# Kernel optimization log

Measured on AMD Instinct MI355X. Metric: run time of the kernel, lower is better.

## Reference

```python
import jax, jax.numpy as jnp
import numpy as np
import math

B, T, D, H = 2, 2048, 1024, 16
DH = D // H          # 64
NB = DH // 2         # 32 rope blocks
EPS = 1e-5


def _layernorm(x, g, b):
    m = jnp.mean(x, axis=-1, keepdims=True)
    v = jnp.var(x, axis=-1, keepdims=True)
    return (x - m) * jax.lax.rsqrt(v + EPS) * g + b


def _rope(x, cos, sin):
    # x: (B,H,T,DH); cos/sin: (B,H,T,NB)
    x1 = x[..., 0::2]
    x2 = x[..., 1::2]
    o1 = x1 * cos - x2 * sin
    o2 = x1 * sin + x2 * cos
    return jnp.stack([o1, o2], axis=-1).reshape(x.shape)


def setup_inputs() -> dict:
    key = jax.random.key(0)
    ks = jax.random.split(key, 16)
    x = jax.random.normal(ks[0], (B, T, D), dtype=jnp.float32)
    # genuine RoPE angles broadcast to (B,H,T,NB)
    inv_freq = 1.0 / (10000.0 ** (np.arange(NB, dtype=np.float32) / NB))
    ang = jnp.asarray(np.arange(T, dtype=np.float32)[:, None] * inv_freq[None, :])  # (T,NB)
    cos_a = jnp.broadcast_to(jnp.cos(ang)[None, None], (B, H, T, NB)).astype(jnp.float32)
    sin_a = jnp.broadcast_to(jnp.sin(ang)[None, None], (B, H, T, NB)).astype(jnp.float32)
    causal_mask = jnp.triu(jnp.ones((T, T), dtype=bool), k=1)  # True above diagonal -> masked
    s = 0.02
    def w(k, shp):
        return jax.random.normal(k, shp, dtype=jnp.float32) * s
    return {
        "x": x, "cos_a": cos_a, "sin_a": sin_a, "causal_mask": causal_mask,
        "Wq": w(ks[1], (D, D)), "bq": jnp.zeros((D,), jnp.float32),
        "Wk": w(ks[2], (D, D)), "bk": jnp.zeros((D,), jnp.float32),
        "Wv": w(ks[3], (D, D)), "bv": jnp.zeros((D,), jnp.float32),
        "Wo": w(ks[4], (D, D)), "bo": jnp.zeros((D,), jnp.float32),
        "g1": jnp.ones((D,), jnp.float32), "b1n": jnp.zeros((D,), jnp.float32),
        "g2": jnp.ones((D,), jnp.float32), "b2n": jnp.zeros((D,), jnp.float32),
        "W1": w(ks[5], (D, 4 * D)), "bf1": jnp.zeros((4 * D,), jnp.float32),
        "W2": w(ks[6], (4 * D, D)), "bf2": jnp.zeros((D,), jnp.float32),
    }


def reference(x, cos_a, sin_a, causal_mask, Wq, bq, Wk, bk, Wv, bv, Wo, bo,
              g1, b1n, g2, b2n, W1, bf1, W2, bf2):
    h = _layernorm(x, g1, b1n)
    def heads(y):
        return y.reshape(B, T, H, DH).transpose(0, 2, 1, 3)  # (B,H,T,DH)
    Q = heads(h @ Wq + bq)
    K = heads(h @ Wk + bk)
    V = heads(h @ Wv + bv)
    Q = _rope(Q, cos_a, sin_a)
    K = _rope(K, cos_a, sin_a)
    scale = math.sqrt(DH)
    scores = jnp.einsum('bhqd,bhkd->bhqk', Q, K) / scale
    scores = jnp.where(causal_mask[None, None], -jnp.inf, scores)
    attn = jax.nn.softmax(scores, axis=-1)
    out = jnp.einsum('bhqk,bhkd->bhqd', attn, V)
    out = out.transpose(0, 2, 1, 3).reshape(B, T, D)
    out = out @ Wo + bo
    x = x + out  # dropout=0.0 (eval)
    h2 = _layernorm(x, g2, b2n)
    ffn = jax.nn.gelu(h2 @ W1 + bf1, approximate=False) @ W2 + bf2
    return x + ffn
```

## Files before the change

### kernel.cpp

```cpp
#include <hip/hip_runtime.h>

typedef unsigned short u16;
typedef unsigned int   u32;
typedef __attribute__((ext_vector_type(8))) short          short8;
typedef __attribute__((ext_vector_type(4))) float          f32x4;
typedef __attribute__((ext_vector_type(8))) unsigned short u16x8;
typedef __attribute__((ext_vector_type(4))) unsigned short u16x4;

#define T_SEQ  2048
#define DMODEL 1024
#define NHEAD  16
#define DHEAD  64
#define HBUF   4194304

__device__ __forceinline__ float bf2f(u16 u) {
    u32 i = ((u32)u) << 16; float f; __builtin_memcpy(&f, &i, 4); return f;
}
__device__ __forceinline__ u16 f2bf(float f) {
    u32 x; __builtin_memcpy(&x, &f, 4);
    return (u16)((x + 0x7FFFu + ((x >> 16) & 1u)) >> 16);
}

__device__ __forceinline__ void gld16(const u16* g, u16* l) {
    auto gp = reinterpret_cast<const __attribute__((address_space(1))) u32*>(
        reinterpret_cast<uintptr_t>(g));
    auto lp = reinterpret_cast<__attribute__((address_space(3))) u32*>(
        (u32)reinterpret_cast<uintptr_t>(l));
    __builtin_amdgcn_global_load_lds(gp, lp, 16, 0, 0);
}

template<int N> __device__ __forceinline__ void wait_vmcnt() {
    if constexpr (N == 0)      asm volatile("s_waitcnt vmcnt(0)" ::: "memory");
    else if constexpr (N == 3) asm volatile("s_waitcnt vmcnt(3)" ::: "memory");
    else                       asm volatile("s_waitcnt vmcnt(4)" ::: "memory");
}

__global__ __launch_bounds__(256) void ln_k(const float* __restrict__ x,
                                            const float* __restrict__ g,
                                            const float* __restrict__ bb,
                                            u16* __restrict__ out)
{
    int row = blockIdx.x, tid = threadIdx.x;
    const float* xr = x + (size_t)row * DMODEL;
    f32x4 v = *(const f32x4*)(xr + tid * 4);
    float s  = v[0] + v[1] + v[2] + v[3];
    float s2 = v[0]*v[0] + v[1]*v[1] + v[2]*v[2] + v[3]*v[3];
    #pragma unroll
    for (int o = 32; o; o >>= 1) { s += __shfl_xor(s, o); s2 += __shfl_xor(s2, o); }
    __shared__ float rs[4], rq[4];
    if ((tid & 63) == 0) { rs[tid >> 6] = s; rq[tid >> 6] = s2; }
    __syncthreads();
    float S  = rs[0] + rs[1] + rs[2] + rs[3];
    float S2 = rq[0] + rq[1] + rq[2] + rq[3];
    float mean = S * (1.f / DMODEL);
    float var  = S2 * (1.f / DMODEL) - mean * mean;
    float rstd = rsqrtf(var + 1e-5f);
    f32x4 gv = *(const f32x4*)(g + tid * 4);
    f32x4 bv = *(const f32x4*)(bb + tid * 4);
    u16x4 o;
    #pragma unroll
    for (int e = 0; e < 4; e++)
        o[e] = f2bf((v[e] - mean) * rstd * gv[e] + bv[e]);
    *(u16x4*)(out + (size_t)row * DMODEL + tid * 4) = o;
}

__device__ __forceinline__ void tr_body(const float* __restrict__ in,
                                        u16* __restrict__ out, int R, int C,
                                        int bx, int by, int tid)
{
    __shared__ u16 s[64][72];
    int c0 = bx * 64, r0 = by * 64;
    #pragma unroll
    for (int p = 0; p < 2; p++) {
        int r = (tid >> 3) + p * 32, cq = (tid & 7) * 8;
        const float* ip = in + (size_t)(r0 + r) * C + c0 + cq;
        f32x4 a = *(const f32x4*)ip;
        f32x4 b = *(const f32x4*)(ip + 4);
        u16x8 o;
        #pragma unroll
        for (int e = 0; e < 4; e++) { o[e] = f2bf(a[e]); o[4 + e] = f2bf(b[e]); }
        *(u16x8*)(&s[r][cq]) = o;
    }
    __syncthreads();
    int oc = tid >> 2, kq = (tid & 3) * 16;
    u16 tmp[16] __attribute__((aligned(16)));
    #pragma unroll
    for (int e = 0; e < 16; e++) tmp[e] = s[kq + e][oc];
    u16* op = out + (size_t)(c0 + oc) * R + r0 + kq;
    *(u16x8*)op       = *(const u16x8*)(&tmp[0]);
    *(u16x8*)(op + 8) = *(const u16x8*)(&tmp[8]);
}

__global__ __launch_bounds__(256) void trall_k(const float* __restrict__ w0, const float* __restrict__ w1,
                                               const float* __restrict__ w2, const float* __restrict__ w3,
                                               const float* __restrict__ wf1, const float* __restrict__ wf2,
                                               u16* __restrict__ o0, u16* __restrict__ o1,
                                               u16* __restrict__ o2, u16* __restrict__ o3,
                                               u16* __restrict__ of1, u16* __restrict__ of2)
{
    int z = blockIdx.z;
    if (z < 4) {
        const float* in = (z == 0) ? w0 : (z == 1) ? w1 : (z == 2) ? w2 : w3;
        u16* out        = (z == 0) ? o0 : (z == 1) ? o1 : (z == 2) ? o2 : o3;
        tr_body(in, out, 1024, 1024, blockIdx.x, blockIdx.y, threadIdx.x);
    } else if (z < 8) {
        tr_body(wf1, of1, 1024, 4096, blockIdx.x + 16 * (z - 4), blockIdx.y, threadIdx.x);
    } else {
        tr_body(wf2, of2, 4096, 1024, blockIdx.x, blockIdx.y + 16 * (z - 8), threadIdx.x);
    }
}

constexpr int EPI_QKV = 0, EPI_RESF = 1, EPI_GELU = 2, EPI_RES2 = 3;

template<int EPI, int BM>
__global__ __launch_bounds__(256) void gemm_k(
    const u16* __restrict__ A, const u16* __restrict__ Bt, void* __restrict__ outv,
    int M, int N, int K, int Kld,
    const float* __restrict__ b0, const float* __restrict__ b1, const float* __restrict__ b2,
    const float* __restrict__ resid,
    const float* __restrict__ cosp, const float* __restrict__ sinp)
{
    constexpr int MI  = BM / 32;
    constexpr int ASZ = BM * 32, BSZ = 128 * 32;
    constexpr int G   = (BM == 128) ? 4 : 3;
    __shared__ u16 As[3 * ASZ];
    __shared__ u16 Bs[3 * BSZ];
    int tid = threadIdx.x;
    int n0 = blockIdx.x * 128, m0 = blockIdx.y * BM;
    int wave = tid >> 6, lane = tid & 63, lm = lane & 15, ko = lane >> 4;
    int wm = (wave & 1) * (BM / 2), wn = (wave >> 1) * 64;
    f32x4 acc[MI][4];
    #pragma unroll
    for (int i = 0; i < MI; i++)
        #pragma unroll
        for (int j = 0; j < 4; j++) acc[i][j] = (f32x4){0.f, 0.f, 0.f, 0.f};

    int srow = wave * 16 + (lane >> 2);
    int scol = (lane & 3) * 8;
    const u16* Ag = A  + (size_t)(m0 + srow) * Kld + scol;
    const u16* Bg = Bt + (size_t)(n0 + srow) * Kld + scol;
    u16* Al = &As[wave * 16 * 32];
    u16* Bl = &Bs[wave * 16 * 32];

    auto issue = [&](int t, int b) {
        u16* Al2 = Al + b * ASZ;
        u16* Bl2 = Bl + b * BSZ;
        const u16* Ag2 = Ag + t * 32;
        const u16* Bg2 = Bg + t * 32;
        gld16(Ag2, Al2);
        if constexpr (BM == 128) gld16(Ag2 + 64 * (size_t)Kld, Al2 + 64 * 32);
        gld16(Bg2,                    Bl2);
        gld16(Bg2 + 64 * (size_t)Kld, Bl2 + 64 * 32);
    };

    int NT = K >> 5;
    issue(0, 0);
    issue(1, 1);

    int bc = 0, bn = 2;
    for (int kt = 0; kt < NT; kt++) {
        if (kt + 1 < NT) wait_vmcnt<G>();
        else             wait_vmcnt<0>();
        __builtin_amdgcn_s_barrier();
        __builtin_amdgcn_sched_barrier(0);
        if (kt + 2 < NT) issue(kt + 2, bn);

        const u16* Ab = &As[bc * ASZ];
        const u16* Bb = &Bs[bc * BSZ];
        short8 af[MI], bf[4];
        #pragma unroll
        for (int i = 0; i < MI; i++) af[i] = *(const short8*)(&Ab[(wm + i * 16 + lm) * 32 + ko * 8]);
        #pragma unroll
        for (int j = 0; j < 4; j++) bf[j] = *(const short8*)(&Bb[(wn + j * 16 + lm) * 32 + ko * 8]);
        __builtin_amdgcn_s_setprio(1);
        #pragma unroll
        for (int i = 0; i < MI; i++)
            #pragma unroll
            for (int j = 0; j < 4; j++)
                acc[i][j] = __builtin_amdgcn_mfma_f32_16x16x32_bf16(af[i], bf[j], acc[i][j], 0, 0, 0);
        __builtin_amdgcn_s_setprio(0);
        bc = (bc == 2) ? 0 : bc + 1;
        bn = (bn == 2) ? 0 : bn + 1;
    }

    #pragma unroll
    for (int i = 0; i < MI; i++) {
        #pragma unroll
        for (int j = 0; j < 4; j++) {
            int n = n0 + wn + j * 16 + lm;
            #pragma unroll
            for (int r = 0; r < 4; r++) {
                int m = m0 + wm + i * 16 + ko * 4 + r;
                float v = acc[i][j][r];
                if constexpr (EPI == EPI_QKV) {
                    int which = n >> 10, nn = n & 1023;
                    const float* bp = (which == 0) ? b0 : (which == 1 ? b1 : b2);
                    v += bp[nn];
                    float vp = __shfl_xor(v, 1);
                    int bi = m >> 11, t2 = m & 2047, hh = nn >> 6, d = nn & 63;
                    u16* outp = (u16*)outv + (size_t)which * HBUF;
                    if (which < 2) {
                        size_t oidx = ((size_t)((bi * NHEAD + hh) * T_SEQ + t2)) * DHEAD + d;
                        size_t ci = ((size_t)((bi * NHEAD + hh) * T_SEQ + t2)) * 32 + (d >> 1);
                        float c = cosp[ci], sn = sinp[ci];
                        float o = (d & 1) ? (vp * sn + v * c) : (v * c - vp * sn);
                        if (which == 0) o *= 0.18033688f;
                        outp[oidx] = f2bf(o);
                    } else {
                        size_t oidx = ((size_t)((bi * NHEAD + hh) * DHEAD + d)) * T_SEQ + t2;
                        outp[oidx] = f2bf(v);
                    }
                } else if constexpr (EPI == EPI_RESF) {
                    v += b0[n] + resid[(size_t)m * N + n];
                    ((float*)outv)[(size_t)m * N + n] = v;
                } else if constexpr (EPI == EPI_GELU) {
                    v += b0[n];
                    float gl = 0.5f * v * (1.f + erff(v * 0.70710678118654752f));
                    ((u16*)outv)[(size_t)m * N + n] = f2bf(gl);
                } else {
                    v += b0[n] + resid[(size_t)m * N + n];
                    ((float*)outv)[(size_t)m * N + n] = v;
                }
            }
        }
    }
}

__device__ __forceinline__ void attn_step(
    bool diag, int wave, int lm, int ko,
    short8 aq0, short8 aq1,
    const u16 (*sK)[72], const u16 (*sV)[72], u16 (*sPw)[72],
    f32x4* oacc, float* lr)
{
    f32x4 sacc[4];
    #pragma unroll
    for (int j = 0; j < 4; j++) {
        short8 bk0 = *(const short8*)(&sK[j * 16 + lm][ko * 8]);
        short8 bk1 = *(const short8*)(&sK[j * 16 + lm][32 + ko * 8]);
        f32x4 z = (f32x4){0.f, 0.f, 0.f, 0.f};
        z = __builtin_amdgcn_mfma_f32_16x16x32_bf16(aq0, bk0, z, 0, 0, 0);
        z = __builtin_amdgcn_mfma_f32_16x16x32_bf16(aq1, bk1, z, 0, 0, 0);
        sacc[j] = z;
    }
    if (diag) {
        #pragma unroll
        for (int j = 0; j < 4; j++)
            #pragma unroll
            for (int r = 0; r < 4; r++)
                if (j * 16 + lm > wave * 16 + ko * 4 + r) sacc[j][r] = -1e30f;
    }

    u16 pb[4][4];
    #pragma unroll
    for (int j = 0; j < 4; j++)
        #pragma unroll
        for (int r = 0; r < 4; r++) {
            float p = __builtin_amdgcn_exp2f(sacc[j][r]);
            lr[r] += p;
            pb[j][r] = f2bf(p);
        }

    #pragma unroll
    for (int j = 0; j < 4; j++)
        #pragma unroll
        for (int r = 0; r < 4; r++) sPw[ko * 4 + r][j * 16 + lm] = pb[j][r];

    #pragma unroll
    for (int ks = 0; ks < 2; ks++) {
        short8 ap = *(const short8*)(&sPw[lm][ks * 32 + ko * 8]);
        #pragma unroll
        for (int j = 0; j < 4; j++) {
            short8 bv = *(const short8*)(&sV[j * 16 + lm][ks * 32 + ko * 8]);
            oacc[j] = __builtin_amdgcn_mfma_f32_16x16x32_bf16(ap, bv, oacc[j], 0, 0, 0);
        }
    }
}

__global__ __launch_bounds__(256) void fattn_k(const u16* __restrict__ Q,
                                               const u16* __restrict__ K,
                                               const u16* __restrict__ Vt,
                                               u16* __restrict__ out)
{
    __shared__ u16 sQP[4][16][72];
    __shared__ u16 sK[2][64][72];
    __shared__ u16 sV[2][64][72];
    int tid = threadIdx.x;
    int qtA = blockIdx.x;
    int qtB = 31 - qtA;
    int bh = blockIdx.y;
    int wave = tid >> 6, lane = tid & 63, lm = lane & 15, ko = lane >> 4;
    int bi = bh >> 4, hh = bh & 15;

    const u16* Kb = K  + (size_t)bh * T_SEQ * DHEAD;
    const u16* Vb = Vt + (size_t)bh * DHEAD * T_SEQ;
    u16* sQf = &sQP[0][0][0];
    int srow = tid >> 2, scol = (tid & 3) * 16;

    short8 aqA0, aqA1, aqB0, aqB1;
    {
        const u16* QbA = Q + ((size_t)bh * T_SEQ + qtA * 64) * DHEAD + (size_t)srow * DHEAD + scol;
        *(u16x8*)(&sQf[srow * 72 + scol])     = *(const u16x8*)QbA;
        *(u16x8*)(&sQf[srow * 72 + scol + 8]) = *(const u16x8*)(QbA + 8);
        __syncthreads();
        aqA0 = *(const short8*)(&sQf[(wave * 16 + lm) * 72 + ko * 8]);
        aqA1 = *(const short8*)(&sQf[(wave * 16 + lm) * 72 + 32 + ko * 8]);
        __syncthreads();
        const u16* QbB = Q + ((size_t)bh * T_SEQ + qtB * 64) * DHEAD + (size_t)srow * DHEAD + scol;
        *(u16x8*)(&sQf[srow * 72 + scol])     = *(const u16x8*)QbB;
        *(u16x8*)(&sQf[srow * 72 + scol + 8]) = *(const u16x8*)(QbB + 8);
        __syncthreads();
        aqB0 = *(const short8*)(&sQf[(wave * 16 + lm) * 72 + ko * 8]);
        aqB1 = *(const short8*)(&sQf[(wave * 16 + lm) * 72 + 32 + ko * 8]);
    }

    f32x4 oA[4], oB[4];
    float lA[4], lB[4];
    #pragma unroll
    for (int j = 0; j < 4; j++) { oA[j] = (f32x4){0,0,0,0}; oB[j] = (f32x4){0,0,0,0}; }
    #pragma unroll
    for (int r = 0; r < 4; r++) { lA[r] = 0.f; lB[r] = 0.f; }

    int nA = qtA + 1, n = nA + qtB + 1;

    u16x8 pk0, pk1, pv0, pv1;
    {
        const u16* kp = Kb + (size_t)srow * DHEAD + scol;
        pk0 = *(const u16x8*)kp; pk1 = *(const u16x8*)(kp + 8);
        const u16* vp = Vb + (size_t)srow * T_SEQ + scol;
        pv0 = *(const u16x8*)vp; pv1 = *(const u16x8*)(vp + 8);
    }

    for (int i = 0; i < n; i++) {
        bool isA = i < nA;
        int kt = isA ? i : i - nA;
        int buf = i & 1;

        *(u16x8*)(&sK[buf][srow][scol])     = pk0;
        *(u16x8*)(&sK[buf][srow][scol + 8]) = pk1;
        *(u16x8*)(&sV[buf][srow][scol])     = pv0;
        *(u16x8*)(&sV[buf][srow][scol + 8]) = pv1;

        if (i + 1 < n) {
            int kt2 = (i + 1 < nA) ? i + 1 : i + 1 - nA;
            const u16* kp = Kb + ((size_t)(kt2 * 64 + srow)) * DHEAD + scol;
            pk0 = *(const u16x8*)kp; pk1 = *(const u16x8*)(kp + 8);
            const u16* vp = Vb + (size_t)srow * T_SEQ + kt2 * 64 + scol;
            pv0 = *(const u16x8*)vp; pv1 = *(const u16x8*)(vp + 8);
        }

        __syncthreads();

        if (isA)
            attn_step(kt == qtA, wave, lm, ko, aqA0, aqA1, sK[buf], sV[buf], sQP[wave], oA, lA);
        else
            attn_step(kt == qtB, wave, lm, ko, aqB0, aqB1, sK[buf], sV[buf], sQP[wave], oB, lB);
    }

    #pragma unroll
    for (int o = 1; o < 16; o <<= 1)
        #pragma unroll
        for (int r = 0; r < 4; r++) { lA[r] += __shfl_xor(lA[r], o); lB[r] += __shfl_xor(lB[r], o); }
    #pragma unroll
    for (int r = 0; r < 4; r++) { lA[r] = 1.f / lA[r]; lB[r] = 1.f / lB[r]; }
    int qrowA = qtA * 64 + wave * 16, qrowB = qtB * 64 + wave * 16;
    #pragma unroll
    for (int j = 0; j < 4; j++)
        #pragma unroll
        for (int r = 0; r < 4; r++) {
            out[((size_t)(bi * T_SEQ) + qrowA + ko * 4 + r) * DMODEL + hh * DHEAD + j * 16 + lm]
                = f2bf(oA[j][r] * lA[r]);
            out[((size_t)(bi * T_SEQ) + qrowB + ko * 4 + r) * DMODEL + hh * DHEAD + j * 16 + lm]
                = f2bf(oB[j][r] * lB[r]);
        }
}

extern "C" void kernel_launch(void* const* d_in, const int* in_sizes, int n_in,
                              void* d_out, int out_size, void* d_ws, size_t ws_size,
                              hipStream_t stream)
{
    (void)in_sizes; (void)n_in; (void)out_size; (void)ws_size;
    const float* x    = (const float*)d_in[0];
    const float* cosp = (const float*)d_in[1];
    const float* sinp = (const float*)d_in[2];
    const float* Wq  = (const float*)d_in[4];
    const float* bq  = (const float*)d_in[5];
    const float* Wk  = (const float*)d_in[6];
    const float* bk  = (const float*)d_in[7];
    const float* Wv  = (const float*)d_in[8];
    const float* bv  = (const float*)d_in[9];
    const float* Wo  = (const float*)d_in[10];
    const float* bo  = (const float*)d_in[11];
    const float* g1  = (const float*)d_in[12];
    const float* b1n = (const float*)d_in[13];
    const float* g2  = (const float*)d_in[14];
    const float* b2n = (const float*)d_in[15];
    const float* W1  = (const float*)d_in[16];
    const float* bf1 = (const float*)d_in[17];
    const float* W2  = (const float*)d_in[18];
    const float* bf2 = (const float*)d_in[19];

    char* ws = (char*)d_ws;
    const size_t MB = 1024 * 1024;
    u16*   qkvT  = (u16*)(ws + 0);
    u16*   WoT   = (u16*)(ws + 6 * MB);
    u16*   W1T   = (u16*)(ws + 8 * MB);
    u16*   W2T   = (u16*)(ws + 16 * MB);
    u16*   h     = (u16*)(ws + 24 * MB);
    u16*   qkvh  = (u16*)(ws + 32 * MB);
    u16*   attnC = (u16*)(ws + 56 * MB);
    float* x2    = (float*)(ws + 64 * MB);
    u16*   ffnh  = (u16*)(ws + 80 * MB);

    trall_k<<<dim3(16, 16, 12), 256, 0, stream>>>(
        Wq, Wk, Wv, Wo, W1, W2,
        qkvT, qkvT + 1 * MB, qkvT + 2 * MB, WoT, W1T, W2T);

    ln_k<<<4096, 256, 0, stream>>>(x, g1, b1n, h);
    gemm_k<EPI_QKV, 128><<<dim3(24, 32), 256, 0, stream>>>(
        h, qkvT, qkvh, 4096, 3072, 1024, 1024, bq, bk, bv, nullptr, cosp, sinp);
    fattn_k<<<dim3(16, 32), 256, 0, stream>>>(qkvh, qkvh + HBUF, qkvh + 2 * HBUF, attnC);
    gemm_k<EPI_RESF, 64><<<dim3(8, 64), 256, 0, stream>>>(
        attnC, WoT, x2, 4096, 1024, 1024, 1024, bo, nullptr, nullptr, x, nullptr, nullptr);
    ln_k<<<4096, 256, 0, stream>>>(x2, g2, b2n, h);
    gemm_k<EPI_GELU, 128><<<dim3(32, 32), 256, 0, stream>>>(
        h, W1T, ffnh, 4096, 4096, 1024, 1024, bf1, nullptr, nullptr, nullptr, nullptr, nullptr);
    gemm_k<EPI_RES2, 64><<<dim3(8, 64), 256, 0, stream>>>(
        ffnh, W2T, (float*)d_out, 4096, 1024, 4096, 4096, bf2, nullptr, nullptr, x2, nullptr, nullptr);
}
```

Before: 404.8 us.

## Add 256x256 tiled 8-wave GEMM with pipelined LDS staging for QKV and FFN1

Adds a new GEMM kernel with 256x256 output tiles, 512 threads, and 128 KB of LDS. It double-buffers K-slices through swizzled LDS using direct global-to-LDS loads, with explicit barriers, waitcnts and raised priority to interleave loads with MFMA quadrants. The QKV and W1/GELU GEMMs switch to it to raise arithmetic intensity and cut global traffic per FLOP. In exchange, fewer blocks are launched (192 and 256 tiles on a 256-CU part), which gives tail and occupancy risk, and the hand-scheduled synchronisation is fragile.

```diff
diff --git a/kernel.cpp b/kernel.cpp
--- a/kernel.cpp
+++ b/kernel.cpp
@@ -6,6 +6,7 @@
 typedef __attribute__((ext_vector_type(4))) float          f32x4;
 typedef __attribute__((ext_vector_type(8))) unsigned short u16x8;
 typedef __attribute__((ext_vector_type(4))) unsigned short u16x4;
+typedef __attribute__((ext_vector_type(4))) u32            u32x4;
 
 #define T_SEQ  2048
 #define DMODEL 1024
@@ -28,6 +29,17 @@
         (u32)reinterpret_cast<uintptr_t>(l));
     __builtin_amdgcn_global_load_lds(gp, lp, 16, 0, 0);
 }
+
+__device__ __forceinline__ short8 dsr128(u32 addr) {
+    u32x4 r;
+    asm volatile("ds_read_b128 %0, %1" : "=&v"(r) : "v"(addr));
+    return __builtin_bit_cast(short8, r);
+}
+
+#define BAR()   { asm volatile("s_barrier" ::: "memory"); __builtin_amdgcn_sched_barrier(0); }
+#define LGKM0() { asm volatile("s_waitcnt lgkmcnt(0)" ::: "memory"); __builtin_amdgcn_sched_barrier(0); }
+#define VMC6()  { asm volatile("s_waitcnt vmcnt(6)" ::: "memory"); }
+#define VMC0()  { asm volatile("s_waitcnt vmcnt(0)" ::: "memory"); }
 
 template<int N> __device__ __forceinline__ void wait_vmcnt() {
     if constexpr (N == 0)      asm volatile("s_waitcnt vmcnt(0)" ::: "memory");
@@ -111,6 +123,160 @@
 }
 
 constexpr int EPI_QKV = 0, EPI_RESF = 1, EPI_GELU = 2, EPI_RES2 = 3;
+
+template<int EPI>
+__global__ __launch_bounds__(512) void gemm256_k(
+    const u16* __restrict__ A, const u16* __restrict__ Bt, void* __restrict__ outv,
+    int M, int N, int K, int Kld,
+    const float* __restrict__ b0, const float* __restrict__ b1, const float* __restrict__ b2,
+    const float* __restrict__ resid,
+    const float* __restrict__ cosp, const float* __restrict__ sinp)
+{
+    (void)M;
+    __shared__ u16 sAB[65536];
+    u16* sA = sAB;
+    u16* sB = sAB + 32768;
+    const int tid = threadIdx.x;
+    const int n0 = blockIdx.x * 256, m0 = blockIdx.y * 256;
+    const int lane = tid & 63, wave = tid >> 6, lm = lane & 15, ko = lane >> 4;
+    const int wm2 = wave >> 2, wn2 = wave & 3;
+
+    f32x4 acc[8][4];
+    #pragma unroll
+    for (int i = 0; i < 8; i++)
+        #pragma unroll
+        for (int j = 0; j < 4; j++) acc[i][j] = (f32x4){0.f, 0.f, 0.f, 0.f};
+
+    const int c8 = ((tid & 7) ^ ((tid >> 3) & 7)) * 8;
+    const int r0s = tid >> 3;
+    const u16* Ab0 = A  + (size_t)(m0 + r0s) * Kld + c8;
+    const u16* Bb0 = Bt + (size_t)(n0 + r0s) * Kld + c8;
+    u16* dA0 = sA + tid * 8;
+    u16* dB0 = sB + tid * 8;
+
+    auto stageA = [&](int ts, int h, int kt) {
+        const u16* s0 = Ab0 + (size_t)(h * 128) * Kld + kt * 64;
+        u16* d = dA0 + (ts * 2 + h) * 8192;
+        gld16(s0,                    d);
+        gld16(s0 + 64 * (size_t)Kld, d + 4096);
+    };
+    auto stageB = [&](int ts, int h, int kt) {
+        const u16* s0 = Bb0 + (size_t)(h * 128) * Kld + kt * 64;
+        u16* d = dB0 + (ts * 2 + h) * 8192;
+        gld16(s0,                    d);
+        gld16(s0 + 64 * (size_t)Kld, d + 4096);
+    };
+
+    const u32 sAb = (u32)(uintptr_t)sA;
+    const u32 sBb = (u32)(uintptr_t)sB;
+    const u32 swz = (u32)((lm & 7) << 4);
+    const u32 co0 = ((u32)(ko * 16)) ^ swz;
+    const u32 co1 = ((u32)(64 + ko * 16)) ^ swz;
+
+    short8 aR[4][2], bR[4][2];
+    auto readA = [&](int ts, int mq) {
+        u32 hb = sAb + (u32)((ts * 2 + wm2) * 16384) + (u32)((mq * 64 + lm) * 128);
+        #pragma unroll
+        for (int i = 0; i < 4; i++) {
+            aR[i][0] = dsr128(hb + i * 2048 + co0);
+            aR[i][1] = dsr128(hb + i * 2048 + co1);
+        }
+    };
+    auto readB = [&](int ts) {
+        u32 hb = sBb + (u32)((ts * 2 + (wn2 >> 1)) * 16384) + (u32)(((wn2 & 1) * 64 + lm) * 128);
+        #pragma unroll
+        for (int j = 0; j < 4; j++) {
+            bR[j][0] = dsr128(hb + j * 2048 + co0);
+            bR[j][1] = dsr128(hb + j * 2048 + co1);
+        }
+    };
+
+#define MMAQ(MQ, NQ) { \
+    __builtin_amdgcn_s_setprio(1); \
+    _Pragma("unroll") \
+    for (int i_ = 0; i_ < 4; i_++) { \
+        _Pragma("unroll") \
+        for (int j_ = 0; j_ < 2; j_++) { \
+            acc[(MQ)*4+i_][(NQ)*2+j_] = __builtin_amdgcn_mfma_f32_16x16x32_bf16( \
+                aR[i_][0], bR[(NQ)*2+j_][0], acc[(MQ)*4+i_][(NQ)*2+j_], 0, 0, 0); \
+            acc[(MQ)*4+i_][(NQ)*2+j_] = __builtin_amdgcn_mfma_f32_16x16x32_bf16( \
+                aR[i_][1], bR[(NQ)*2+j_][1], acc[(MQ)*4+i_][(NQ)*2+j_], 0, 0, 0); \
+        } } \
+    __builtin_amdgcn_s_setprio(0); }
+
+    const int NI = K >> 7;
+    stageB(0, 0, 0); stageB(0, 1, 0); stageA(0, 0, 0); stageA(0, 1, 0);
+    stageB(1, 0, 1); stageB(1, 1, 1); stageA(1, 0, 1);
+    VMC6(); BAR();
+
+    for (int t = 0; t < NI; ++t) {
+        const int c1 = 2 * t + 1, x0 = 2 * t + 2, x1 = 2 * t + 3;
+        const bool sn = (t + 1 < NI);
+        readA(0, 0); readB(0);
+        stageA(1, 1, c1);
+        BAR(); LGKM0(); MMAQ(0, 0); BAR();
+        if (sn) stageB(0, 0, x0);
+        BAR(); MMAQ(0, 1); BAR();
+        readA(0, 1);
+        if (sn) stageB(0, 1, x0);
+        BAR(); LGKM0(); MMAQ(1, 0); BAR();
+        if (sn) { stageA(0, 0, x0); VMC6(); } else { VMC0(); }
+        BAR(); MMAQ(1, 1); BAR();
+        readA(1, 0); readB(1);
+        if (sn) stageA(0, 1, x0);
+        BAR(); LGKM0(); MMAQ(0, 0); BAR();
+        if (sn) stageB(1, 0, x1);
+        BAR(); MMAQ(0, 1); BAR();
+        readA(1, 1);
+        if (sn) stageB(1, 1, x1);
+        BAR(); LGKM0(); MMAQ(1, 0); BAR();
+        if (sn) { stageA(1, 0, x1); VMC6(); }
+        BAR(); MMAQ(1, 1); BAR();
+    }
+#undef MMAQ
+
+    #pragma unroll
+    for (int i = 0; i < 8; i++) {
+        #pragma unroll
+        for (int j = 0; j < 4; j++) {
+            int n = n0 + wn2 * 64 + j * 16 + lm;
+            #pragma unroll
+            for (int r = 0; r < 4; r++) {
+                int m = m0 + wm2 * 128 + i * 16 + ko * 4 + r;
+                float v = acc[i][j][r];
+                if constexpr (EPI == EPI_QKV) {
+                    int which = n >> 10, nn = n & 1023;
+                    const float* bp = (which == 0) ? b0 : (which == 1 ? b1 : b2);
+                    v += bp[nn];
+                    float vp = __shfl_xor(v, 1);
+                    int bi = m >> 11, t2 = m & 2047, hh = nn >> 6, d = nn & 63;
+                    u16* outp = (u16*)outv + (size_t)which * HBUF;
+                    if (which < 2) {
+                        size_t oidx = ((size_t)((bi * NHEAD + hh) * T_SEQ + t2)) * DHEAD + d;
+                        size_t ci = ((size_t)((bi * NHEAD + hh) * T_SEQ + t2)) * 32 + (d >> 1);
+                        float c = cosp[ci], sn2 = sinp[ci];
+                        float o = (d & 1) ? (vp * sn2 + v * c) : (v * c - vp * sn2);
+                        if (which == 0) o *= 0.18033688f;
+                        outp[oidx] = f2bf(o);
+                    } else {
+                        size_t oidx = ((size_t)((bi * NHEAD + hh) * DHEAD + d)) * T_SEQ + t2;
+                        outp[oidx] = f2bf(v);
+                    }
+                } else if constexpr (EPI == EPI_RESF) {
+                    v += b0[n] + resid[(size_t)m * N + n];
+                    ((float*)outv)[(size_t)m * N + n] = v;
+                } else if constexpr (EPI == EPI_GELU) {
+                    v += b0[n];
+                    float gl = 0.5f * v * (1.f + erff(v * 0.70710678118654752f));
+                    ((u16*)outv)[(size_t)m * N + n] = f2bf(gl);
+                } else {
+                    v += b0[n] + resid[(size_t)m * N + n];
+                    ((float*)outv)[(size_t)m * N + n] = v;
+                }
+            }
+        }
+    }
+}
 
 template<int EPI, int BM>
 __global__ __launch_bounds__(256) void gemm_k(
@@ -416,13 +582,13 @@
         qkvT, qkvT + 1 * MB, qkvT + 2 * MB, WoT, W1T, W2T);
 
     ln_k<<<4096, 256, 0, stream>>>(x, g1, b1n, h);
-    gemm_k<EPI_QKV, 128><<<dim3(24, 32), 256, 0, stream>>>(
+    gemm256_k<EPI_QKV><<<dim3(12, 16), 512, 0, stream>>>(
         h, qkvT, qkvh, 4096, 3072, 1024, 1024, bq, bk, bv, nullptr, cosp, sinp);
     fattn_k<<<dim3(16, 32), 256, 0, stream>>>(qkvh, qkvh + HBUF, qkvh + 2 * HBUF, attnC);
     gemm_k<EPI_RESF, 64><<<dim3(8, 64), 256, 0, stream>>>(
         attnC, WoT, x2, 4096, 1024, 1024, 1024, bo, nullptr, nullptr, x, nullptr, nullptr);
     ln_k<<<4096, 256, 0, stream>>>(x2, g2, b2n, h);
-    gemm_k<EPI_GELU, 128><<<dim3(32, 32), 256, 0, stream>>>(
+    gemm256_k<EPI_GELU><<<dim3(16, 16), 512, 0, stream>>>(
         h, W1T, ffnh, 4096, 4096, 1024, 1024, bf1, nullptr, nullptr, nullptr, nullptr, nullptr);
     gemm_k<EPI_RES2, 64><<<dim3(8, 64), 256, 0, stream>>>(
         ffnh, W2T, (float*)d_out, 4096, 1024, 4096, 4096, bf2, nullptr, nullptr, x2, nullptr, nullptr);
```

Result: slower. 467.5 us (+15.5%).

## Add 256x256 512-thread GEMM for QKV/FFN1, XCD swizzle, larger Wo/FFN2 tiles

Applied to the files above, without the earlier changes.

Adds a new 512-thread GEMM kernel with 256x256 output tiles and double-buffered LDS, used for the QKV and FFN-up projections. The larger tiles raise data reuse per loaded byte. A block-index swizzle spreads neighbouring tiles across the XCDs for better L2 locality. The Wo and FFN-down GEMMs move from 64-row to 128-row tiles. The catch is that the QKV and FFN-up GEMMs now launch far fewer blocks (192 and 256) on a 256-CU part, so the GPU may be underfilled, and the 256x256 tile uses more registers.

```diff
diff --git a/kernel.cpp b/kernel.cpp
--- a/kernel.cpp
+++ b/kernel.cpp
@@ -33,6 +33,14 @@
     if constexpr (N == 0)      asm volatile("s_waitcnt vmcnt(0)" ::: "memory");
     else if constexpr (N == 3) asm volatile("s_waitcnt vmcnt(3)" ::: "memory");
     else                       asm volatile("s_waitcnt vmcnt(4)" ::: "memory");
+}
+
+__device__ __forceinline__ void xcd_swz(int& bx, int& by) {
+    int gx = gridDim.x;
+    int nwg = gx * gridDim.y;
+    int w = by * gx + bx;
+    int L = (w & 7) * (nwg >> 3) + (w >> 3);
+    bx = L % gx; by = L / gx;
 }
 
 __global__ __launch_bounds__(256) void ln_k(const float* __restrict__ x,
@@ -112,6 +120,122 @@
 
 constexpr int EPI_QKV = 0, EPI_RESF = 1, EPI_GELU = 2, EPI_RES2 = 3;
 
+template<int EPI>
+__device__ __forceinline__ void epi_elem(
+    float v, int m, int n, int N, void* outv,
+    const float* b0, const float* b1, const float* b2,
+    const float* resid, const float* cosp, const float* sinp)
+{
+    if constexpr (EPI == EPI_QKV) {
+        int which = n >> 10, nn = n & 1023;
+        const float* bp = (which == 0) ? b0 : (which == 1 ? b1 : b2);
+        v += bp[nn];
+        float vp = __shfl_xor(v, 1);
+        int bi = m >> 11, t2 = m & 2047, hh = nn >> 6, d = nn & 63;
+        u16* outp = (u16*)outv + (size_t)which * HBUF;
+        if (which < 2) {
+            size_t oidx = ((size_t)((bi * NHEAD + hh) * T_SEQ + t2)) * DHEAD + d;
+            size_t ci = ((size_t)((bi * NHEAD + hh) * T_SEQ + t2)) * 32 + (d >> 1);
+            float c = cosp[ci], sn2 = sinp[ci];
+            float o = (d & 1) ? (vp * sn2 + v * c) : (v * c - vp * sn2);
+            if (which == 0) o *= 0.18033688f;
+            outp[oidx] = f2bf(o);
+        } else {
+            size_t oidx = ((size_t)((bi * NHEAD + hh) * DHEAD + d)) * T_SEQ + t2;
+            outp[oidx] = f2bf(v);
+        }
+    } else if constexpr (EPI == EPI_RESF) {
+        v += b0[n] + resid[(size_t)m * N + n];
+        ((float*)outv)[(size_t)m * N + n] = v;
+    } else if constexpr (EPI == EPI_GELU) {
+        v += b0[n];
+        float gl = 0.5f * v * (1.f + erff(v * 0.70710678118654752f));
+        ((u16*)outv)[(size_t)m * N + n] = f2bf(gl);
+    } else {
+        v += b0[n] + resid[(size_t)m * N + n];
+        ((float*)outv)[(size_t)m * N + n] = v;
+    }
+}
+
+template<int EPI>
+__global__ __launch_bounds__(512) void gemm512_k(
+    const u16* __restrict__ A, const u16* __restrict__ Bt, void* __restrict__ outv,
+    int M, int N, int K, int Kld,
+    const float* __restrict__ b0, const float* __restrict__ b1, const float* __restrict__ b2,
+    const float* __restrict__ resid,
+    const float* __restrict__ cosp, const float* __restrict__ sinp)
+{
+    (void)M;
+    constexpr int TSZ = 256 * 32;
+    __shared__ u16 As[2 * TSZ];
+    __shared__ u16 Bs[2 * TSZ];
+    int tid = threadIdx.x;
+    int bx = blockIdx.x, by = blockIdx.y;
+    xcd_swz(bx, by);
+    int n0 = bx * 256, m0 = by * 256;
+    int wave = tid >> 6, lane = tid & 63, lm = lane & 15, ko = lane >> 4;
+    int wm2 = wave >> 2, wn2 = wave & 3;
+
+    f32x4 acc[8][4];
+    #pragma unroll
+    for (int i = 0; i < 8; i++)
+        #pragma unroll
+        for (int j = 0; j < 4; j++) acc[i][j] = (f32x4){0.f, 0.f, 0.f, 0.f};
+
+    int srow = tid >> 2;
+    int scol = (tid & 3) * 8;
+    const u16* Ag = A  + (size_t)(m0 + srow) * Kld + scol;
+    const u16* Bg = Bt + (size_t)(n0 + srow) * Kld + scol;
+    u16* Alw = &As[wave * 512];
+    u16* Blw = &Bs[wave * 512];
+
+    auto issue = [&](int kt, int b) {
+        const u16* Ag2 = Ag + kt * 32;
+        const u16* Bg2 = Bg + kt * 32;
+        u16* Al2 = Alw + b * TSZ;
+        u16* Bl2 = Blw + b * TSZ;
+        gld16(Ag2,                     Al2);
+        gld16(Ag2 + 128 * (size_t)Kld, Al2 + 4096);
+        gld16(Bg2,                     Bl2);
+        gld16(Bg2 + 128 * (size_t)Kld, Bl2 + 4096);
+    };
+
+    int NT = K >> 5;
+    issue(0, 0);
+    for (int kt = 0; kt < NT; kt++) {
+        __syncthreads();
+        if (kt + 1 < NT) issue(kt + 1, (kt + 1) & 1);
+        const u16* Ab = &As[(kt & 1) * TSZ];
+        const u16* Bb = &Bs[(kt & 1) * TSZ];
+        short8 af[8], bf[4];
+        #pragma unroll
+        for (int i = 0; i < 8; i++)
+            af[i] = *(const short8*)(&Ab[(wm2 * 128 + i * 16 + lm) * 32 + ko * 8]);
+        #pragma unroll
+        for (int j = 0; j < 4; j++)
+            bf[j] = *(const short8*)(&Bb[(wn2 * 64 + j * 16 + lm) * 32 + ko * 8]);
+        __builtin_amdgcn_s_setprio(1);
+        #pragma unroll
+        for (int i = 0; i < 8; i++)
+            #pragma unroll
+            for (int j = 0; j < 4; j++)
+                acc[i][j] = __builtin_amdgcn_mfma_f32_16x16x32_bf16(af[i], bf[j], acc[i][j], 0, 0, 0);
+        __builtin_amdgcn_s_setprio(0);
+    }
+
+    #pragma unroll
+    for (int i = 0; i < 8; i++)
+        #pragma unroll
+        for (int j = 0; j < 4; j++) {
+            int n = n0 + wn2 * 64 + j * 16 + lm;
+            #pragma unroll
+            for (int r = 0; r < 4; r++) {
+                int m = m0 + wm2 * 128 + i * 16 + ko * 4 + r;
+                epi_elem<EPI>(acc[i][j][r], m, n, N, outv, b0, b1, b2, resid, cosp, sinp);
+            }
+        }
+}
+
 template<int EPI, int BM>
 __global__ __launch_bounds__(256) void gemm_k(
     const u16* __restrict__ A, const u16* __restrict__ Bt, void* __restrict__ outv,
@@ -126,7 +250,9 @@
     __shared__ u16 As[3 * ASZ];
     __shared__ u16 Bs[3 * BSZ];
     int tid = threadIdx.x;
-    int n0 = blockIdx.x * 128, m0 = blockIdx.y * BM;
+    int bx = blockIdx.x, by = blockIdx.y;
+    xcd_swz(bx, by);
+    int n0 = bx * 128, m0 = by * BM;
     int wave = tid >> 6, lane = tid & 63, lm = lane & 15, ko = lane >> 4;
     int wm = (wave & 1) * (BM / 2), wn = (wave >> 1) * 64;
     f32x4 acc[MI][4];
@@ -184,46 +310,16 @@
     }
 
     #pragma unroll
-    for (int i = 0; i < MI; i++) {
+    for (int i = 0; i < MI; i++)
         #pragma unroll
         for (int j = 0; j < 4; j++) {
             int n = n0 + wn + j * 16 + lm;
             #pragma unroll
             for (int r = 0; r < 4; r++) {
                 int m = m0 + wm + i * 16 + ko * 4 + r;
-                float v = acc[i][j][r];
-                if constexpr (EPI == EPI_QKV) {
-                    int which = n >> 10, nn = n & 1023;
-                    const float* bp = (which == 0) ? b0 : (which == 1 ? b1 : b2);
-                    v += bp[nn];
-                    float vp = __shfl_xor(v, 1);
-                    int bi = m >> 11, t2 = m & 2047, hh = nn >> 6, d = nn & 63;
-                    u16* outp = (u16*)outv + (size_t)which * HBUF;
-                    if (which < 2) {
-                        size_t oidx = ((size_t)((bi * NHEAD + hh) * T_SEQ + t2)) * DHEAD + d;
-                        size_t ci = ((size_t)((bi * NHEAD + hh) * T_SEQ + t2)) * 32 + (d >> 1);
-                        float c = cosp[ci], sn = sinp[ci];
-                        float o = (d & 1) ? (vp * sn + v * c) : (v * c - vp * sn);
-                        if (which == 0) o *= 0.18033688f;
-                        outp[oidx] = f2bf(o);
-                    } else {
-                        size_t oidx = ((size_t)((bi * NHEAD + hh) * DHEAD + d)) * T_SEQ + t2;
-                        outp[oidx] = f2bf(v);
-                    }
-                } else if constexpr (EPI == EPI_RESF) {
-                    v += b0[n] + resid[(size_t)m * N + n];
-                    ((float*)outv)[(size_t)m * N + n] = v;
-                } else if constexpr (EPI == EPI_GELU) {
-                    v += b0[n];
-                    float gl = 0.5f * v * (1.f + erff(v * 0.70710678118654752f));
-                    ((u16*)outv)[(size_t)m * N + n] = f2bf(gl);
-                } else {
-                    v += b0[n] + resid[(size_t)m * N + n];
-                    ((float*)outv)[(size_t)m * N + n] = v;
-                }
+                epi_elem<EPI>(acc[i][j][r], m, n, N, outv, b0, b1, b2, resid, cosp, sinp);
             }
         }
-    }
 }
 
 __device__ __forceinline__ void attn_step(
@@ -416,14 +512,14 @@
         qkvT, qkvT + 1 * MB, qkvT + 2 * MB, WoT, W1T, W2T);
 
     ln_k<<<4096, 256, 0, stream>>>(x, g1, b1n, h);
-    gemm_k<EPI_QKV, 128><<<dim3(24, 32), 256, 0, stream>>>(
+    gemm512_k<EPI_QKV><<<dim3(12, 16), 512, 0, stream>>>(
         h, qkvT, qkvh, 4096, 3072, 1024, 1024, bq, bk, bv, nullptr, cosp, sinp);
     fattn_k<<<dim3(16, 32), 256, 0, stream>>>(qkvh, qkvh + HBUF, qkvh + 2 * HBUF, attnC);
-    gemm_k<EPI_RESF, 64><<<dim3(8, 64), 256, 0, stream>>>(
+    gemm_k<EPI_RESF, 128><<<dim3(8, 32), 256, 0, stream>>>(
         attnC, WoT, x2, 4096, 1024, 1024, 1024, bo, nullptr, nullptr, x, nullptr, nullptr);
     ln_k<<<4096, 256, 0, stream>>>(x2, g2, b2n, h);
-    gemm_k<EPI_GELU, 128><<<dim3(32, 32), 256, 0, stream>>>(
+    gemm512_k<EPI_GELU><<<dim3(16, 16), 512, 0, stream>>>(
         h, W1T, ffnh, 4096, 4096, 1024, 1024, bf1, nullptr, nullptr, nullptr, nullptr, nullptr);
-    gemm_k<EPI_RES2, 64><<<dim3(8, 64), 256, 0, stream>>>(
+    gemm_k<EPI_RES2, 128><<<dim3(8, 32), 256, 0, stream>>>(
         ffnh, W2T, (float*)d_out, 4096, 1024, 4096, 4096, bf2, nullptr, nullptr, x2, nullptr, nullptr);
 }
```

Result: slower. 427.7 us (+5.7%).
